# Kernel tuning notes

Measured on AMD Instinct MI355X. Metric: run time of the kernel, lower is better.

The kernel has to match this reference:

```python
import jax, jax.numpy as jnp
import numpy as np

B, S, D_MODEL = 2, 2048, 2048
N_HEADS, N_KV_HEADS = 32, 8
HEAD_DIM = D_MODEL // N_HEADS  # 64


def setup_inputs() -> dict:
    key = jax.random.key(0)
    ks = jax.random.split(key, 7)
    # rope frequencies (as in standard RoPE; values just need to be the right shape)
    inv_freq = 1.0 / (10000.0 ** (jnp.arange(0, HEAD_DIM, 2, dtype=jnp.float32) / HEAD_DIM))
    t = jnp.arange(S, dtype=jnp.float32)
    freqs = t[:, None] * inv_freq[None, :]  # (S, head_dim//2)
    scale = 0.02
    return {
        "x": jax.random.normal(ks[0], (B, S, D_MODEL), jnp.float32),
        "cos": jnp.cos(freqs),
        "sin": jnp.sin(freqs),
        "Wq": jax.random.normal(ks[1], (N_HEADS * HEAD_DIM, D_MODEL), jnp.float32) * scale,
        "Wk": jax.random.normal(ks[2], (N_KV_HEADS * HEAD_DIM, D_MODEL), jnp.float32) * scale,
        "Wv": jax.random.normal(ks[3], (N_KV_HEADS * HEAD_DIM, D_MODEL), jnp.float32) * scale,
        "Wo": jax.random.normal(ks[4], (D_MODEL, D_MODEL), jnp.float32) * scale,
    }


def _apply_rope(x, cos, sin):
    # x: (B, H, S, D); cos/sin: (S, D//2)
    d = x.shape[-1]
    x1, x2 = x[..., : d // 2], x[..., d // 2:]
    c = cos[None, None]
    s = sin[None, None]
    return jnp.concatenate([x1 * c - x2 * s, x1 * s + x2 * c], axis=-1)


def reference(x, cos, sin, Wq, Wk, Wv, Wo):
    b, s, _ = x.shape
    hd = 2 * cos.shape[-1]
    h = Wq.shape[0] // hd
    kv = Wk.shape[0] // hd
    g = h // kv  # query heads per kv head

    q = (x @ Wq.T).reshape(b, s, h, hd).transpose(0, 2, 1, 3)    # (b,h,s,d)
    k = (x @ Wk.T).reshape(b, s, kv, hd).transpose(0, 2, 1, 3)   # (b,kv,s,d)
    v = (x @ Wv.T).reshape(b, s, kv, hd).transpose(0, 2, 1, 3)

    q = _apply_rope(q, cos, sin)
    k = _apply_rope(k, cos, sin)

    # GQA: group query heads instead of materializing repeated K/V
    qg = q.reshape(b, kv, g, s, hd)
    scale = 1.0 / jnp.sqrt(jnp.asarray(hd, x.dtype))
    scores = jnp.einsum('bkgsd,bktd->bkgst', qg, k) * scale      # (b,kv,g,s,s)
    causal = jnp.arange(s)[:, None] >= jnp.arange(s)[None, :]
    scores = jnp.where(causal[None, None, None], scores, jnp.asarray(-jnp.inf, scores.dtype))
    attn = jax.nn.softmax(scores, axis=-1)
    out = jnp.einsum('bkgst,bktd->bkgsd', attn, v)               # (b,kv,g,s,d)
    out = out.reshape(b, h, s, hd).transpose(0, 2, 1, 3).reshape(b, s, h * hd)
    return out @ Wo.T
```

## Files before the change

kernel.cpp:

```cpp
#include <hip/hip_runtime.h>
#include <hip/hip_bf16.h>

typedef __bf16 bf16;
typedef __attribute__((ext_vector_type(8))) __bf16 bf16x8;
typedef __attribute__((ext_vector_type(4))) __bf16 bf16x4;
typedef __attribute__((ext_vector_type(4))) float f32x4;

#define B_SZ 2
#define S_SZ 2048
#define D_SZ 2048
#define H_SZ 32
#define KV_SZ 8
#define HD_SZ 64
#define M_SZ (B_SZ * S_SZ)
#define NQKV 3072

#define GLDS(g, s) __builtin_amdgcn_global_load_lds( \
    (const __attribute__((address_space(1))) void*)(g), \
    (__attribute__((address_space(3))) void*)(s), 16, 0, 0)

__device__ __forceinline__ void bar_lgkm() {
    asm volatile("s_waitcnt lgkmcnt(0)\n\ts_barrier" ::: "memory");
}

__global__ void cvt_all(const float* __restrict__ x, const float* __restrict__ Wq,
                        const float* __restrict__ Wk, const float* __restrict__ Wv,
                        const float* __restrict__ Wo,
                        bf16* __restrict__ xb, bf16* __restrict__ Wf, bf16* __restrict__ wob,
                        int nx, int n1, int n2) {
    int i = blockIdx.x * blockDim.x + threadIdx.x;
    const float* src; bf16* dst; int off;
    if (i < nx)                 { src = x;  dst = xb; off = i; }
    else {
        int j = i - nx;
        if (j < n1)             { src = Wq; dst = Wf; off = j; }
        else if (j < n1 + n2)   { src = Wk; dst = Wf + (size_t)4 * n1; off = j - n1; }
        else if (j < n1 + 2*n2) { src = Wv; dst = Wf + (size_t)4 * (n1 + n2); off = j - n1 - n2; }
        else if (j < 2*n1+2*n2) { src = Wo; dst = wob; off = j - n1 - 2 * n2; }
        else return;
    }
    float4 v = ((const float4*)src)[off];
    bf16x4 o;
    o.x = (bf16)v.x; o.y = (bf16)v.y; o.z = (bf16)v.z; o.w = (bf16)v.w;
    ((bf16x4*)dst)[off] = o;
}

#define GEMM_CORE4(A_, B_, Kdim)                                                 \
    const int tid  = threadIdx.x;                                                \
    const int wv   = tid >> 6;                                                   \
    const int lane = tid & 63;                                                   \
    const int c = lane & 15, quad = lane >> 4;                                   \
    const int wr = wv >> 1, wc = wv & 1;                                         \
    const int g8 = lane >> 3;                                                    \
    const int chs = ((lane & 7) ^ g8) * 8;                                       \
    const int rowBase = blockIdx.y * 128;                                        \
    const int colBase = blockIdx.x * 128;                                        \
    const bf16* Ag = A_ + (size_t)(rowBase + wv * 32 + g8) * Kdim + chs;         \
    const bf16* Bg = B_ + (size_t)(colBase + wv * 32 + g8) * Kdim + chs;         \
    bf16* sAw = As + (wv * 32) * 64;                                             \
    bf16* sBw = Bs + (wv * 32) * 64;                                             \
    f32x4 acc[4][4] = {};                                                        \
    for (int k0 = 0; k0 < Kdim; k0 += 64) {                                      \
        _Pragma("unroll")                                                        \
        for (int j = 0; j < 4; j++) {                                            \
            GLDS(Ag + (size_t)(j * 8) * Kdim + k0, sAw + j * 512);               \
            GLDS(Bg + (size_t)(j * 8) * Kdim + k0, sBw + j * 512);               \
        }                                                                        \
        __syncthreads();                                                         \
        _Pragma("unroll")                                                        \
        for (int ks = 0; ks < 2; ks++) {                                         \
            bf16x8 af[4], bfr[4];                                                \
            _Pragma("unroll")                                                    \
            for (int mi = 0; mi < 4; mi++)                                       \
                af[mi] = *(const bf16x8*)(As + (wr * 64 + mi * 16 + c) * 64      \
                                          + (((ks << 2) + quad) ^ (c & 7)) * 8); \
            _Pragma("unroll")                                                    \
            for (int ni = 0; ni < 4; ni++)                                       \
                bfr[ni] = *(const bf16x8*)(Bs + (wc * 64 + ni * 16 + c) * 64     \
                                          + (((ks << 2) + quad) ^ (c & 7)) * 8); \
            _Pragma("unroll")                                                    \
            for (int mi = 0; mi < 4; mi++)                                       \
                _Pragma("unroll")                                                \
                for (int ni = 0; ni < 4; ni++)                                   \
                    acc[mi][ni] = __builtin_amdgcn_mfma_f32_16x16x32_bf16(       \
                        af[mi], bfr[ni], acc[mi][ni], 0, 0, 0);                  \
        }                                                                        \
        __syncthreads();                                                         \
    }                                                                            \
    const int mBase = rowBase + wr * 64;                                         \
    const int nBase = colBase + wc * 64;

__global__ __launch_bounds__(256, 2)
void gemm_qkv(const bf16* __restrict__ A, const bf16* __restrict__ Bw,
              bf16* __restrict__ Qb, bf16* __restrict__ Kb, bf16* __restrict__ Vtb,
              const float* __restrict__ cosp, const float* __restrict__ sinp,
              float qscale)
{
    __shared__ __align__(16) bf16 As[128 * 64];
    __shared__ __align__(16) bf16 Bs[128 * 64];

    GEMM_CORE4(A, Bw, D_SZ)

    const int hcol = nBase;
    if (hcol < 2560) {
        bf16* dst; int hh, Hn; float sc;
        if (hcol < 2048) { dst = Qb; hh = hcol >> 6;        Hn = H_SZ;  sc = qscale; }
        else             { dst = Kb; hh = (hcol >> 6) - 32; Hn = KV_SZ; sc = 1.0f;  }
#pragma unroll
        for (int mi = 0; mi < 4; mi++) {
#pragma unroll
            for (int r = 0; r < 4; r++) {
                int row = mBase + mi * 16 + quad * 4 + r;
                int b = row >> 11;
                int s = row & 2047;
                const float* cr = cosp + (size_t)s * 32;
                const float* sr = sinp + (size_t)s * 32;
                size_t base = ((size_t)(b * Hn + hh) * S_SZ + s) * 64;
#pragma unroll
                for (int nj = 0; nj < 2; nj++) {
                    int d = nj * 16 + c;
                    float x1 = acc[mi][nj][r];
                    float x2 = acc[mi][nj + 2][r];
                    float cv = cr[d], sv = sr[d];
                    dst[base + d]      = (bf16)((x1 * cv - x2 * sv) * sc);
                    dst[base + d + 32] = (bf16)((x1 * sv + x2 * cv) * sc);
                }
            }
        }
    } else {
        const int kvh = (hcol >> 6) - 40;
        const int b   = mBase >> 11;
        const int s0  = mBase & 2047;
#pragma unroll
        for (int nj = 0; nj < 4; nj++) {
            int d = nj * 16 + c;
            size_t base = ((size_t)(b * KV_SZ + kvh) * 64 + d) * (size_t)S_SZ;
#pragma unroll
            for (int mi = 0; mi < 4; mi++) {
                int s = s0 + mi * 16 + quad * 4;
#pragma unroll
                for (int r = 0; r < 4; r++)
                    Vtb[base + s + r] = (bf16)acc[mi][nj][r];
            }
        }
    }
}

__global__ __launch_bounds__(256, 2)
void gemm_out(const bf16* __restrict__ A, const bf16* __restrict__ Bw,
              float* __restrict__ Co, int N, int K)
{
    __shared__ __align__(16) bf16 As[128 * 64];
    __shared__ __align__(16) bf16 Bs[128 * 64];

    GEMM_CORE4(A, Bw, K)

#pragma unroll
    for (int mi = 0; mi < 4; mi++)
#pragma unroll
        for (int ni = 0; ni < 4; ni++) {
            int col = nBase + ni * 16 + c;
#pragma unroll
            for (int r = 0; r < 4; r++) {
                int row = mBase + mi * 16 + quad * 4 + r;
                Co[(size_t)row * N + col] = acc[mi][ni][r];
            }
        }
}

#define PST 72

__global__ __launch_bounds__(256, 3)
void flash_attn(const bf16* __restrict__ Q, const bf16* __restrict__ Kc,
                const bf16* __restrict__ Vt, bf16* __restrict__ Aout)
{
    __shared__ __align__(16) bf16 Ks[64 * 64];
    __shared__ __align__(16) bf16 Vs[64 * 64];
    __shared__ __align__(16) bf16 Ps[2 * 4 * 16 * PST];

    const int tid  = threadIdx.x;
    const int lane = tid & 63;
    const int wave = tid >> 6;
    const int c = lane & 15, quad = lane >> 4;
    const int qloc = wave * 16 + c;

    const int i  = (blockIdx.x + blockIdx.y) & 15;
    const int tA = 31 - i, tB = i;
    const int q0A = tA << 6, q0B = tB << 6;

    const int bh = blockIdx.y;
    const int b  = bh >> 5;
    const int h  = bh & 31;
    const int kv = h >> 2;

    const bf16* Qp = Q  + (size_t)bh * (S_SZ * 64);
    const bf16* Kp = Kc + (size_t)(b * KV_SZ + kv) * (S_SZ * 64);
    const bf16* Vp = Vt + (size_t)(b * KV_SZ + kv) * (64 * S_SZ);

    bf16x8 aqA[2], aqB[2];
    {
        const bf16* qa = Qp + (size_t)(q0A + qloc) * 64 + quad * 8;
        aqA[0] = *(const bf16x8*)qa;  aqA[1] = *(const bf16x8*)(qa + 32);
        const bf16* qb = Qp + (size_t)(q0B + qloc) * 64 + quad * 8;
        aqB[0] = *(const bf16x8*)qb;  aqB[1] = *(const bf16x8*)(qb + 32);
    }

    f32x4 oA[4] = {}, oB[4] = {};
    f32x4 lA = {}, lB = {};

    bf16x8 ones;
#pragma unroll
    for (int j = 0; j < 8; j++) ones[j] = (bf16)1.0f;

    const int srow = tid >> 3;
    const int ch   = tid & 7;
    const int sws  = (ch ^ (srow & 7)) * 8;
    const bf16* Kg0 = Kp + (size_t)srow * 64 + ch * 8;
    const bf16* Kg1 = Kp + (size_t)(srow + 32) * 64 + ch * 8;
    const bf16* Vg0 = Vp + (size_t)srow * S_SZ + ch * 8;
    const bf16* Vg1 = Vp + (size_t)(srow + 32) * S_SZ + ch * 8;

    uint4 pk0 = *(const uint4*)Kg0, pk1 = *(const uint4*)Kg1;
    uint4 pv0 = *(const uint4*)Vg0, pv1 = *(const uint4*)Vg1;

    bf16* PwA = Ps + wave * 16 * PST;
    bf16* PwB = Ps + (4 + wave) * 16 * PST;

    for (int kt = 0; kt <= tA; kt++) {
        *(uint4*)(Ks + srow * 64 + sws)        = pk0;
        *(uint4*)(Ks + (srow + 32) * 64 + sws) = pk1;
        *(uint4*)(Vs + srow * 64 + sws)        = pv0;
        *(uint4*)(Vs + (srow + 32) * 64 + sws) = pv1;
        if (kt < tA) {
            pk0 = *(const uint4*)(Kg0 + (size_t)(kt + 1) * 4096);
            pk1 = *(const uint4*)(Kg1 + (size_t)(kt + 1) * 4096);
            pv0 = *(const uint4*)(Vg0 + (kt + 1) * 64);
            pv1 = *(const uint4*)(Vg1 + (kt + 1) * 64);
        }
        bar_lgkm();

        const bool doB   = (kt <= tB);
        const bool diagA = (kt == tA);
        const bool diagB = (kt == tB);

        f32x4 scA[4] = {}, scB[4] = {};
#pragma unroll
        for (int ks = 0; ks < 2; ks++) {
            bf16x8 ak4[4];
#pragma unroll
            for (int ni = 0; ni < 4; ni++)
                ak4[ni] = *(const bf16x8*)(Ks + (ni * 16 + c) * 64
                                           + (((ks << 2) + quad) ^ (c & 7)) * 8);
            __builtin_amdgcn_s_setprio(1);
#pragma unroll
            for (int ni = 0; ni < 4; ni++)
                scA[ni] = __builtin_amdgcn_mfma_f32_16x16x32_bf16(ak4[ni], aqA[ks], scA[ni], 0, 0, 0);
            if (doB) {
#pragma unroll
                for (int ni = 0; ni < 4; ni++)
                    scB[ni] = __builtin_amdgcn_mfma_f32_16x16x32_bf16(ak4[ni], aqB[ks], scB[ni], 0, 0, 0);
            }
            __builtin_amdgcn_s_setprio(0);
        }

        if (diagA) {
#pragma unroll
            for (int ni = 0; ni < 4; ni++) {
                bf16x4 pk;
#pragma unroll
                for (int r = 0; r < 4; r++) {
                    float p = exp2f(scA[ni][r]);
                    if ((ni * 16 + quad * 4 + r) > qloc) p = 0.f;
                    pk[r] = (bf16)p;
                }
                *(bf16x4*)(PwA + c * PST + ni * 16 + quad * 4) = pk;
            }
        } else {
#pragma unroll
            for (int ni = 0; ni < 4; ni++) {
                bf16x4 pk;
#pragma unroll
                for (int r = 0; r < 4; r++) pk[r] = (bf16)exp2f(scA[ni][r]);
                *(bf16x4*)(PwA + c * PST + ni * 16 + quad * 4) = pk;
            }
        }
        if (doB) {
            if (diagB) {
#pragma unroll
                for (int ni = 0; ni < 4; ni++) {
                    bf16x4 pk;
#pragma unroll
                    for (int r = 0; r < 4; r++) {
                        float p = exp2f(scB[ni][r]);
                        if ((ni * 16 + quad * 4 + r) > qloc) p = 0.f;
                        pk[r] = (bf16)p;
                    }
                    *(bf16x4*)(PwB + c * PST + ni * 16 + quad * 4) = pk;
                }
            } else {
#pragma unroll
                for (int ni = 0; ni < 4; ni++) {
                    bf16x4 pk;
#pragma unroll
                    for (int r = 0; r < 4; r++) pk[r] = (bf16)exp2f(scB[ni][r]);
                    *(bf16x4*)(PwB + c * PST + ni * 16 + quad * 4) = pk;
                }
            }
        }

#pragma unroll
        for (int ks = 0; ks < 2; ks++) {
            bf16x8 av4[4];
#pragma unroll
            for (int ni = 0; ni < 4; ni++)
                av4[ni] = *(const bf16x8*)(Vs + (ni * 16 + c) * 64
                                           + (((ks << 2) + quad) ^ (c & 7)) * 8);
            bf16x8 bpA = *(const bf16x8*)(PwA + c * PST + ks * 32 + quad * 8);
            __builtin_amdgcn_s_setprio(1);
            lA = __builtin_amdgcn_mfma_f32_16x16x32_bf16(ones, bpA, lA, 0, 0, 0);
#pragma unroll
            for (int ni = 0; ni < 4; ni++)
                oA[ni] = __builtin_amdgcn_mfma_f32_16x16x32_bf16(av4[ni], bpA, oA[ni], 0, 0, 0);
            __builtin_amdgcn_s_setprio(0);
            if (doB) {
                bf16x8 bpB = *(const bf16x8*)(PwB + c * PST + ks * 32 + quad * 8);
                __builtin_amdgcn_s_setprio(1);
                lB = __builtin_amdgcn_mfma_f32_16x16x32_bf16(ones, bpB, lB, 0, 0, 0);
#pragma unroll
                for (int ni = 0; ni < 4; ni++)
                    oB[ni] = __builtin_amdgcn_mfma_f32_16x16x32_bf16(av4[ni], bpB, oB[ni], 0, 0, 0);
                __builtin_amdgcn_s_setprio(0);
            }
        }
        bar_lgkm();
    }

    {
        float ila = 1.f / lA[0];
        float ilb = 1.f / lB[0];
        bf16* pa = Aout + ((size_t)(b * S_SZ + q0A + qloc)) * D_SZ + h * 64;
        bf16* pb = Aout + ((size_t)(b * S_SZ + q0B + qloc)) * D_SZ + h * 64;
#pragma unroll
        for (int ni = 0; ni < 4; ni++) {
            bf16x4 wa, wb;
#pragma unroll
            for (int r = 0; r < 4; r++) {
                wa[r] = (bf16)(oA[ni][r] * ila);
                wb[r] = (bf16)(oB[ni][r] * ilb);
            }
            *(bf16x4*)(pa + ni * 16 + quad * 4) = wa;
            *(bf16x4*)(pb + ni * 16 + quad * 4) = wb;
        }
    }
}

extern "C" void kernel_launch(void* const* d_in, const int* in_sizes, int n_in,
                              void* d_out, int out_size, void* d_ws, size_t ws_size,
                              hipStream_t stream) {
    const float* x    = (const float*)d_in[0];
    const float* cosp = (const float*)d_in[1];
    const float* sinp = (const float*)d_in[2];
    const float* Wq   = (const float*)d_in[3];
    const float* Wk   = (const float*)d_in[4];
    const float* Wv   = (const float*)d_in[5];
    const float* Wo   = (const float*)d_in[6];
    float* out = (float*)d_out;

    const int M = M_SZ;
    const int D = D_SZ;
    const int NKV = KV_SZ * HD_SZ;

    bf16* xb   = (bf16*)d_ws;
    bf16* Wf   = xb  + (size_t)M * D;
    bf16* Qb   = Wf  + (size_t)NQKV * D;
    bf16* Kb   = Qb  + (size_t)M * D;
    bf16* Vtb  = Kb  + (size_t)B_SZ * KV_SZ * S_SZ * 64;
    bf16* wob  = Vtb + (size_t)B_SZ * KV_SZ * 64 * S_SZ;
    bf16* attn = xb;

    const int nx = M * D / 4, n1 = D * D / 4, n2 = NKV * D / 4;

    cvt_all<<<(nx + 2 * n1 + 2 * n2 + 255) / 256, 256, 0, stream>>>(
        x, Wq, Wk, Wv, Wo, xb, Wf, wob, nx, n1, n2);

    const float qscale = 0.125f * 1.44269504089f;

    gemm_qkv<<<dim3(NQKV / 128, M / 128), 256, 0, stream>>>(xb, Wf, Qb, Kb, Vtb, cosp, sinp, qscale);

    flash_attn<<<dim3(16, B_SZ * H_SZ), 256, 0, stream>>>(Qb, Kb, Vtb, attn);

    gemm_out<<<dim3(D / 128, M / 128), 256, 0, stream>>>(attn, wob, out, D, D);
}
```

Baseline: 294.7 us.

## Keep softmax probabilities in registers and use 16x16x16 MFMA for PV

The probability tile is no longer written to LDS and reloaded. The score accumulator layout is fed straight into PV via 16x16x16 bf16 MFMAs, which match the register layout. K/V LDS tiles switch from XOR swizzle to a padded stride of 72, and occupancy launch bounds drop from 3 to 2. This removes LDS traffic and its latency for P, but uses more, smaller MFMA instructions with lower per-instruction throughput.

```diff
diff --git a/kernel.cpp b/kernel.cpp
--- a/kernel.cpp
+++ b/kernel.cpp
@@ -5,6 +5,7 @@
 typedef __attribute__((ext_vector_type(8))) __bf16 bf16x8;
 typedef __attribute__((ext_vector_type(4))) __bf16 bf16x4;
 typedef __attribute__((ext_vector_type(4))) float f32x4;
+typedef __attribute__((ext_vector_type(4))) short short4v;
 
 #define B_SZ 2
 #define S_SZ 2048
@@ -21,6 +22,21 @@
 
 __device__ __forceinline__ void bar_lgkm() {
     asm volatile("s_waitcnt lgkmcnt(0)\n\ts_barrier" ::: "memory");
+}
+
+#if defined(__has_builtin)
+#if __has_builtin(__builtin_amdgcn_mfma_f32_16x16x16bf16_1k)
+#define HAVE_MFMA16 1
+#endif
+#endif
+__device__ __forceinline__ f32x4 mfma16(bf16x4 a, bf16x4 b, f32x4 c) {
+#ifdef HAVE_MFMA16
+    return __builtin_amdgcn_mfma_f32_16x16x16bf16_1k(
+        __builtin_bit_cast(short4v, a), __builtin_bit_cast(short4v, b), c, 0, 0, 0);
+#else
+    asm("v_mfma_f32_16x16x16_bf16 %0, %1, %2, %0" : "+v"(c) : "v"(a), "v"(b));
+    return c;
+#endif
 }
 
 __global__ void cvt_all(const float* __restrict__ x, const float* __restrict__ Wq,
@@ -168,15 +184,14 @@
         }
 }
 
-#define PST 72
-
-__global__ __launch_bounds__(256, 3)
+#define KVST 72
+
+__global__ __launch_bounds__(256, 2)
 void flash_attn(const bf16* __restrict__ Q, const bf16* __restrict__ Kc,
                 const bf16* __restrict__ Vt, bf16* __restrict__ Aout)
 {
-    __shared__ __align__(16) bf16 Ks[64 * 64];
-    __shared__ __align__(16) bf16 Vs[64 * 64];
-    __shared__ __align__(16) bf16 Ps[2 * 4 * 16 * PST];
+    __shared__ __align__(16) bf16 Ks[64 * KVST];
+    __shared__ __align__(16) bf16 Vs[64 * KVST];
 
     const int tid  = threadIdx.x;
     const int lane = tid & 63;
@@ -208,13 +223,12 @@
     f32x4 oA[4] = {}, oB[4] = {};
     f32x4 lA = {}, lB = {};
 
-    bf16x8 ones;
-#pragma unroll
-    for (int j = 0; j < 8; j++) ones[j] = (bf16)1.0f;
+    bf16x4 ones4;
+#pragma unroll
+    for (int j = 0; j < 4; j++) ones4[j] = (bf16)1.0f;
 
     const int srow = tid >> 3;
     const int ch   = tid & 7;
-    const int sws  = (ch ^ (srow & 7)) * 8;
     const bf16* Kg0 = Kp + (size_t)srow * 64 + ch * 8;
     const bf16* Kg1 = Kp + (size_t)(srow + 32) * 64 + ch * 8;
     const bf16* Vg0 = Vp + (size_t)srow * S_SZ + ch * 8;
@@ -223,14 +237,11 @@
     uint4 pk0 = *(const uint4*)Kg0, pk1 = *(const uint4*)Kg1;
     uint4 pv0 = *(const uint4*)Vg0, pv1 = *(const uint4*)Vg1;
 
-    bf16* PwA = Ps + wave * 16 * PST;
-    bf16* PwB = Ps + (4 + wave) * 16 * PST;
-
     for (int kt = 0; kt <= tA; kt++) {
-        *(uint4*)(Ks + srow * 64 + sws)        = pk0;
-        *(uint4*)(Ks + (srow + 32) * 64 + sws) = pk1;
-        *(uint4*)(Vs + srow * 64 + sws)        = pv0;
-        *(uint4*)(Vs + (srow + 32) * 64 + sws) = pv1;
+        *(uint4*)(Ks + srow * KVST + ch * 8)        = pk0;
+        *(uint4*)(Ks + (srow + 32) * KVST + ch * 8) = pk1;
+        *(uint4*)(Vs + srow * KVST + ch * 8)        = pv0;
+        *(uint4*)(Vs + (srow + 32) * KVST + ch * 8) = pv1;
         if (kt < tA) {
             pk0 = *(const uint4*)(Kg0 + (size_t)(kt + 1) * 4096);
             pk1 = *(const uint4*)(Kg1 + (size_t)(kt + 1) * 4096);
@@ -249,8 +260,8 @@
             bf16x8 ak4[4];
 #pragma unroll
             for (int ni = 0; ni < 4; ni++)
-                ak4[ni] = *(const bf16x8*)(Ks + (ni * 16 + c) * 64
-                                           + (((ks << 2) + quad) ^ (c & 7)) * 8);
+                ak4[ni] = *(const bf16x8*)(Ks + (ni * 16 + c) * KVST
+                                           + ((ks << 2) + quad) * 8);
             __builtin_amdgcn_s_setprio(1);
 #pragma unroll
             for (int ni = 0; ni < 4; ni++)
@@ -263,74 +274,59 @@
             __builtin_amdgcn_s_setprio(0);
         }
 
+        bf16x4 pA[4], pB[4];
         if (diagA) {
 #pragma unroll
-            for (int ni = 0; ni < 4; ni++) {
-                bf16x4 pk;
+            for (int ni = 0; ni < 4; ni++)
 #pragma unroll
                 for (int r = 0; r < 4; r++) {
                     float p = exp2f(scA[ni][r]);
                     if ((ni * 16 + quad * 4 + r) > qloc) p = 0.f;
-                    pk[r] = (bf16)p;
+                    pA[ni][r] = (bf16)p;
                 }
-                *(bf16x4*)(PwA + c * PST + ni * 16 + quad * 4) = pk;
-            }
         } else {
 #pragma unroll
-            for (int ni = 0; ni < 4; ni++) {
-                bf16x4 pk;
-#pragma unroll
-                for (int r = 0; r < 4; r++) pk[r] = (bf16)exp2f(scA[ni][r]);
-                *(bf16x4*)(PwA + c * PST + ni * 16 + quad * 4) = pk;
-            }
+            for (int ni = 0; ni < 4; ni++)
+#pragma unroll
+                for (int r = 0; r < 4; r++) pA[ni][r] = (bf16)exp2f(scA[ni][r]);
         }
         if (doB) {
             if (diagB) {
 #pragma unroll
-                for (int ni = 0; ni < 4; ni++) {
-                    bf16x4 pk;
+                for (int ni = 0; ni < 4; ni++)
 #pragma unroll
                     for (int r = 0; r < 4; r++) {
                         float p = exp2f(scB[ni][r]);
                         if ((ni * 16 + quad * 4 + r) > qloc) p = 0.f;
-                        pk[r] = (bf16)p;
+                        pB[ni][r] = (bf16)p;
                     }
-                    *(bf16x4*)(PwB + c * PST + ni * 16 + quad * 4) = pk;
-                }
             } else {
 #pragma unroll
-                for (int ni = 0; ni < 4; ni++) {
-                    bf16x4 pk;
-#pragma unroll
-                    for (int r = 0; r < 4; r++) pk[r] = (bf16)exp2f(scB[ni][r]);
-                    *(bf16x4*)(PwB + c * PST + ni * 16 + quad * 4) = pk;
-                }
-            }
-        }
-
-#pragma unroll
-        for (int ks = 0; ks < 2; ks++) {
-            bf16x8 av4[4];
-#pragma unroll
-            for (int ni = 0; ni < 4; ni++)
-                av4[ni] = *(const bf16x8*)(Vs + (ni * 16 + c) * 64
-                                           + (((ks << 2) + quad) ^ (c & 7)) * 8);
-            bf16x8 bpA = *(const bf16x8*)(PwA + c * PST + ks * 32 + quad * 8);
+                for (int ni = 0; ni < 4; ni++)
+#pragma unroll
+                    for (int r = 0; r < 4; r++) pB[ni][r] = (bf16)exp2f(scB[ni][r]);
+            }
+        }
+
+#pragma unroll
+        for (int dblk = 0; dblk < 4; dblk++) {
+            bf16x4 vf[4];
+#pragma unroll
+            for (int kb = 0; kb < 4; kb++)
+                vf[kb] = *(const bf16x4*)(Vs + (dblk * 16 + c) * KVST
+                                          + kb * 16 + quad * 4);
             __builtin_amdgcn_s_setprio(1);
-            lA = __builtin_amdgcn_mfma_f32_16x16x32_bf16(ones, bpA, lA, 0, 0, 0);
-#pragma unroll
-            for (int ni = 0; ni < 4; ni++)
-                oA[ni] = __builtin_amdgcn_mfma_f32_16x16x32_bf16(av4[ni], bpA, oA[ni], 0, 0, 0);
+#pragma unroll
+            for (int kb = 0; kb < 4; kb++) {
+                oA[dblk] = mfma16(vf[kb], pA[kb], oA[dblk]);
+                if (doB) oB[dblk] = mfma16(vf[kb], pB[kb], oB[dblk]);
+            }
             __builtin_amdgcn_s_setprio(0);
-            if (doB) {
-                bf16x8 bpB = *(const bf16x8*)(PwB + c * PST + ks * 32 + quad * 8);
-                __builtin_amdgcn_s_setprio(1);
-                lB = __builtin_amdgcn_mfma_f32_16x16x32_bf16(ones, bpB, lB, 0, 0, 0);
-#pragma unroll
-                for (int ni = 0; ni < 4; ni++)
-                    oB[ni] = __builtin_amdgcn_mfma_f32_16x16x32_bf16(av4[ni], bpB, oB[ni], 0, 0, 0);
-                __builtin_amdgcn_s_setprio(0);
-            }
+        }
+#pragma unroll
+        for (int kb = 0; kb < 4; kb++) {
+            lA = mfma16(ones4, pA[kb], lA);
+            if (doB) lB = mfma16(ones4, pB[kb], lB);
         }
         bar_lgkm();
     }
```

New measurement: 295.1 us. Within noise of the previous version (+0.2%).

## Double-buffer LDS tiles in GEMM core to prefetch next K-slice

Applied to the files above, without the earlier changes.

Converts the shared GEMM core to a two-stage LDS ping-pong: the next 64-wide K tile is issued via global_load_lds before computing on the current one. Explicit vmcnt waits let the current tile land while the next is in flight, so global-load latency can hide behind MFMA work. LDS per block doubles to 64 KB, which may limit the occupancy targeted by launch_bounds(256,2).

```diff
diff --git a/kernel.cpp b/kernel.cpp
--- a/kernel.cpp
+++ b/kernel.cpp
@@ -45,7 +45,7 @@
     ((bf16x4*)dst)[off] = o;
 }
 
-#define GEMM_CORE4(A_, B_, Kdim)                                                 \
+#define GEMM_CORE5(A_, B_, Kdim)                                                 \
     const int tid  = threadIdx.x;                                                \
     const int wv   = tid >> 6;                                                   \
     const int lane = tid & 63;                                                   \
@@ -57,26 +57,39 @@
     const int colBase = blockIdx.x * 128;                                        \
     const bf16* Ag = A_ + (size_t)(rowBase + wv * 32 + g8) * Kdim + chs;         \
     const bf16* Bg = B_ + (size_t)(colBase + wv * 32 + g8) * Kdim + chs;         \
-    bf16* sAw = As + (wv * 32) * 64;                                             \
-    bf16* sBw = Bs + (wv * 32) * 64;                                             \
     f32x4 acc[4][4] = {};                                                        \
+    _Pragma("unroll")                                                            \
+    for (int j = 0; j < 4; j++) {           \
+        GLDS(Ag + (size_t)(j * 8) * Kdim, Ls + (wv * 32 + j * 8) * 64);          \
+        GLDS(Bg + (size_t)(j * 8) * Kdim, Ls + 8192 + (wv * 32 + j * 8) * 64);   \
+    }                                                                            \
     for (int k0 = 0; k0 < Kdim; k0 += 64) {                                      \
-        _Pragma("unroll")                                                        \
-        for (int j = 0; j < 4; j++) {                                            \
-            GLDS(Ag + (size_t)(j * 8) * Kdim + k0, sAw + j * 512);               \
-            GLDS(Bg + (size_t)(j * 8) * Kdim + k0, sBw + j * 512);               \
+        bf16* Asb = Ls + ((k0 >> 6) & 1) * 16384;                                \
+        bf16* Bsb = Asb + 8192;                                                  \
+        if (k0 + 64 < Kdim) {                \
+            bf16* Asn = Ls + ((((k0 >> 6) & 1) ^ 1) * 16384);                    \
+            _Pragma("unroll")                                                    \
+            for (int j = 0; j < 4; j++) {                                        \
+                GLDS(Ag + (size_t)(j * 8) * Kdim + (k0 + 64),                    \
+                     Asn + (wv * 32 + j * 8) * 64);                              \
+                GLDS(Bg + (size_t)(j * 8) * Kdim + (k0 + 64),                    \
+                     Asn + 8192 + (wv * 32 + j * 8) * 64);                       \
+            }                                                                    \
+            asm volatile("s_waitcnt vmcnt(8)" ::: "memory");                     \
+        } else {                                                                 \
+            asm volatile("s_waitcnt vmcnt(0)" ::: "memory");                     \
         }                                                                        \
-        __syncthreads();                                                         \
+        asm volatile("s_waitcnt lgkmcnt(0)\n\ts_barrier" ::: "memory");          \
         _Pragma("unroll")                                                        \
         for (int ks = 0; ks < 2; ks++) {                                         \
             bf16x8 af[4], bfr[4];                                                \
             _Pragma("unroll")                                                    \
             for (int mi = 0; mi < 4; mi++)                                       \
-                af[mi] = *(const bf16x8*)(As + (wr * 64 + mi * 16 + c) * 64      \
+                af[mi] = *(const bf16x8*)(Asb + (wr * 64 + mi * 16 + c) * 64     \
                                           + (((ks << 2) + quad) ^ (c & 7)) * 8); \
             _Pragma("unroll")                                                    \
             for (int ni = 0; ni < 4; ni++)                                       \
-                bfr[ni] = *(const bf16x8*)(Bs + (wc * 64 + ni * 16 + c) * 64     \
+                bfr[ni] = *(const bf16x8*)(Bsb + (wc * 64 + ni * 16 + c) * 64    \
                                           + (((ks << 2) + quad) ^ (c & 7)) * 8); \
             _Pragma("unroll")                                                    \
             for (int mi = 0; mi < 4; mi++)                                       \
@@ -85,7 +98,7 @@
                     acc[mi][ni] = __builtin_amdgcn_mfma_f32_16x16x32_bf16(       \
                         af[mi], bfr[ni], acc[mi][ni], 0, 0, 0);                  \
         }                                                                        \
-        __syncthreads();                                                         \
+        asm volatile("s_waitcnt lgkmcnt(0)\n\ts_barrier" ::: "memory");          \
     }                                                                            \
     const int mBase = rowBase + wr * 64;                                         \
     const int nBase = colBase + wc * 64;
@@ -96,10 +109,9 @@
               const float* __restrict__ cosp, const float* __restrict__ sinp,
               float qscale)
 {
-    __shared__ __align__(16) bf16 As[128 * 64];
-    __shared__ __align__(16) bf16 Bs[128 * 64];
-
-    GEMM_CORE4(A, Bw, D_SZ)
+    __shared__ __align__(16) bf16 Ls[2 * 16384];
+
+    GEMM_CORE5(A, Bw, D_SZ)
 
     const int hcol = nBase;
     if (hcol < 2560) {
@@ -150,10 +162,9 @@
 void gemm_out(const bf16* __restrict__ A, const bf16* __restrict__ Bw,
               float* __restrict__ Co, int N, int K)
 {
-    __shared__ __align__(16) bf16 As[128 * 64];
-    __shared__ __align__(16) bf16 Bs[128 * 64];
-
-    GEMM_CORE4(A, Bw, K)
+    __shared__ __align__(16) bf16 Ls[2 * 16384];
+
+    GEMM_CORE5(A, Bw, K)
 
 #pragma unroll
     for (int mi = 0; mi < 4; mi++)
```

New measurement: 276.8 us. -6.1%, faster.
